# Kernel optimization log

Measured on AMD Instinct MI355X. Metric: run time of the kernel, lower is better.

The kernel has to match this reference:

```python
import jax, jax.numpy as jnp
import numpy as np

B, S, D = 1, 2048, 2048
E, K, F = 16, 4, 512
EPS = 1e-6


def setup_inputs() -> dict:
    key = jax.random.key(0)
    ks = jax.random.split(key, 5)
    return {
        "hidden_states": jax.random.normal(ks[0], (B, S, D), dtype=jnp.float32),
        "norm_weight": jnp.ones((D,), dtype=jnp.float32),
        "gate_w": jax.random.normal(ks[1], (E, D), dtype=jnp.float32) * 0.02,
        "w_gate": jax.random.normal(ks[2], (E, D, F), dtype=jnp.float32) * 0.02,
        "w_up": jax.random.normal(ks[3], (E, D, F), dtype=jnp.float32) * 0.02,
        "w_down": jax.random.normal(ks[4], (E, F, D), dtype=jnp.float32) * 0.02,
    }


def _rmsnorm(x, w, eps=EPS):
    xf = x.astype(jnp.float32)
    var = jnp.mean(xf * xf, axis=-1, keepdims=True)
    return (xf * jax.lax.rsqrt(var + eps)).astype(x.dtype) * w


def reference(hidden_states, norm_weight, gate_w, w_gate, w_up, w_down):
    residual = hidden_states
    h = _rmsnorm(hidden_states, norm_weight)
    x = h.reshape(-1, D)                                  # [T, D], T = B*S
    T = x.shape[0]

    # Router: softmax over experts (fp32), top-k, renormalize top-k weights.
    logits = x @ gate_w.T                                  # [T, E]
    probs = jax.nn.softmax(logits.astype(jnp.float32), axis=-1)
    top_w, top_i = jax.lax.top_k(probs, K)                 # [T, K]
    top_w = top_w / jnp.sum(top_w, axis=-1, keepdims=True)
    top_w = top_w.astype(x.dtype)

    # Dense combine matrix [T, E]: routing weight if selected, else 0.
    comb = jnp.zeros((T, E), dtype=x.dtype)
    comb = comb.at[jnp.arange(T)[:, None], top_i].add(top_w)

    # Experts: SiLU-gated MLP per expert, combined with routing weights.
    g = jnp.einsum("td,edf->tef", x, w_gate)               # [T, E, F]
    u = jnp.einsum("td,edf->tef", x, w_up)                 # [T, E, F]
    act = jax.nn.silu(g) * u                               # [T, E, F]
    # Weight per-expert contributions then project down.
    y = jnp.einsum("tef,efd,te->td", act, w_down, comb)    # [T, D]

    out = residual + y.reshape(B, S, D)
    return out
```

## Files before the change

kernel.cpp:

```cpp
#include <hip/hip_runtime.h>
#include <cstdint>
#include <cstddef>

#define T_ 2048
#define D_ 2048
#define E_ 16
#define F_ 512

typedef unsigned short u16;
typedef unsigned int u32;
typedef unsigned long long u64;
typedef __attribute__((ext_vector_type(8))) short bf16x8;
typedef __attribute__((ext_vector_type(4))) float f32x4;
typedef __attribute__((ext_vector_type(2))) u32 u32x2;
typedef __attribute__((ext_vector_type(8))) u16 u16x8;
typedef __attribute__((ext_vector_type(4))) u16 u16x4;

__device__ __forceinline__ u16 f2bf(float f){
  union { float f; u32 u; } c; c.f = f;
  return (u16)((c.u + 0x7FFFu + ((c.u >> 16) & 1u)) >> 16);
}

__device__ __forceinline__ void gload16(const void* g, void* l){
  __builtin_amdgcn_global_load_lds((const __attribute__((address_space(1))) void*)g,
                                   (__attribute__((address_space(3))) void*)l,
                                   16, 0, 0);
}

__device__ __forceinline__ void st4(u16* p, float4 v){
  u32 lo, hi;
  asm("v_cvt_pk_bf16_f32 %0, %1, %2" : "=v"(lo) : "v"(v.x), "v"(v.y));
  asm("v_cvt_pk_bf16_f32 %0, %1, %2" : "=v"(hi) : "v"(v.z), "v"(v.w));
  u32x2 u = {lo, hi};
  *(u32x2*)p = u;
}

__global__ __launch_bounds__(256) void k_transpose_cast(
    const float* __restrict__ src, u16* __restrict__ dst, int R, int C)
{
  const int e = blockIdx.z;
  const int r0 = blockIdx.y * 64, c0 = blockIdx.x * 64;
  const int tid = threadIdx.x;
  __shared__ __align__(16) u16 tile[64][68];
  const float* s = src + ((size_t)e * R + r0) * C + c0;
  const int ir = tid >> 4, jc = (tid & 15) * 4;
  #pragma unroll
  for (int q = 0; q < 4; ++q){
    const int i = ir + q*16;
    const float4 v = *(const float4*)(s + (size_t)i * C + jc);
    st4(&tile[i][jc], v);
  }
  __syncthreads();
  u16* d = dst + ((size_t)e * C + c0) * R + r0;
  #pragma unroll
  for (int q = 0; q < 4; ++q){
    const int a = ir + q*16;
    u16x4 pkt = { tile[jc+0][a], tile[jc+1][a], tile[jc+2][a], tile[jc+3][a] };
    *(u16x4*)(d + (size_t)a * R + jc) = pkt;
  }
}

__global__ __launch_bounds__(256) void k_norm_router(
    const float* __restrict__ x, const float* __restrict__ nw, const float* __restrict__ gw,
    u16* __restrict__ h, int* __restrict__ tok_e, float* __restrict__ tok_w)
{
  const int t = blockIdx.x, tid = threadIdx.x;
  const int lane = tid & 63, wid = tid >> 6;
  const int d0 = tid * 8;
  const float4 v0 = *(const float4*)(x + (size_t)t*D_ + d0);
  const float4 v1 = *(const float4*)(x + (size_t)t*D_ + d0 + 4);
  float hv[8] = {v0.x, v0.y, v0.z, v0.w, v1.x, v1.y, v1.z, v1.w};
  float ss = 0.f;
  #pragma unroll
  for (int j = 0; j < 8; ++j) ss += hv[j]*hv[j];
  #pragma unroll
  for (int o = 32; o; o >>= 1) ss += __shfl_xor(ss, o);
  __shared__ float sred[4];
  __shared__ float red16[4][16];
  __shared__ float lf[16];
  if (lane == 0) sred[wid] = ss;
  __syncthreads();
  const float rstd = rsqrtf((sred[0]+sred[1]+sred[2]+sred[3]) * (1.f/(float)D_) + 1e-6f);
  const float4 w0 = *(const float4*)(nw + d0);
  const float4 w1 = *(const float4*)(nw + d0 + 4);
  const float wv[8] = {w0.x,w0.y,w0.z,w0.w,w1.x,w1.y,w1.z,w1.w};
  #pragma unroll
  for (int j = 0; j < 8; ++j) hv[j] = hv[j] * rstd * wv[j];
  u16x8 hb;
  #pragma unroll
  for (int j = 0; j < 8; ++j) hb[j] = f2bf(hv[j]);
  *(u16x8*)(h + (size_t)t*D_ + d0) = hb;

  float lg[16];
  #pragma unroll
  for (int e = 0; e < 16; ++e){
    const float4 g0 = *(const float4*)(gw + e*D_ + d0);
    const float4 g1 = *(const float4*)(gw + e*D_ + d0 + 4);
    lg[e] = hv[0]*g0.x + hv[1]*g0.y + hv[2]*g0.z + hv[3]*g0.w
          + hv[4]*g1.x + hv[5]*g1.y + hv[6]*g1.z + hv[7]*g1.w;
  }
  #pragma unroll
  for (int e = 0; e < 16; ++e){
    #pragma unroll
    for (int o = 32; o; o >>= 1) lg[e] += __shfl_xor(lg[e], o);
  }
  if (lane == 0){
    #pragma unroll
    for (int e = 0; e < 16; ++e) red16[wid][e] = lg[e];
  }
  __syncthreads();
  if (tid < 16) lf[tid] = red16[0][tid] + red16[1][tid] + red16[2][tid] + red16[3][tid];
  __syncthreads();
  if (tid == 0){
    float l[16];
    #pragma unroll
    for (int e = 0; e < 16; ++e) l[e] = lf[e];
    int sel[4]; float sv[4]; u32 used = 0;
    for (int k = 0; k < 4; ++k){
      float b = -3.4e38f; int bi = 0;
      for (int e = 0; e < 16; ++e)
        if (!((used >> e) & 1u) && l[e] > b){ b = l[e]; bi = e; }
      used |= 1u << bi; sel[k] = bi; sv[k] = b;
    }
    float ex[4]; float s = 0.f;
    for (int k = 0; k < 4; ++k){ ex[k] = __expf(sv[k] - sv[0]); s += ex[k]; }
    const float inv = 1.f / s;
    int4 te = {sel[0], sel[1], sel[2], sel[3]};
    float4 tw4 = {ex[0]*inv, ex[1]*inv, ex[2]*inv, ex[3]*inv};
    *(int4*)(tok_e + t*4) = te;
    *(float4*)(tok_w + t*4) = tw4;
  }
}

__global__ __launch_bounds__(256) void k_build_lists(
    const int* __restrict__ tok_e, const float* __restrict__ tok_w,
    int* __restrict__ eidx, float* __restrict__ ew, int* __restrict__ counts)
{
  const int e = blockIdx.x, tid = threadIdx.x;
  const int lane = tid & 63, wid = tid >> 6;
  __shared__ int wtot[4];
  __shared__ int base;
  if (tid == 0) base = 0;
  __syncthreads();
  for (int t0 = 0; t0 < T_; t0 += 256){
    const int t = t0 + tid;
    const int4 te = *(const int4*)(tok_e + t*4);
    const float4 tw = *(const float4*)(tok_w + t*4);
    bool m = false; float wv = 0.f;
    if      (te.x == e){ m = true; wv = tw.x; }
    else if (te.y == e){ m = true; wv = tw.y; }
    else if (te.z == e){ m = true; wv = tw.z; }
    else if (te.w == e){ m = true; wv = tw.w; }
    const u64 mask = __ballot(m);
    const int pre = __popcll(mask & ((1ull << lane) - 1ull));
    if (lane == 0) wtot[wid] = __popcll(mask);
    __syncthreads();
    int wbase = base;
    for (int i = 0; i < wid; ++i) wbase += wtot[i];
    if (m){
      eidx[e*T_ + wbase + pre] = t;
      ew[e*T_ + wbase + pre] = wv;
    }
    __syncthreads();
    if (tid == 0) base += wtot[0] + wtot[1] + wtot[2] + wtot[3];
    __syncthreads();
  }
  if (tid == 0) counts[e] = base;
}

__global__ __launch_bounds__(256) void k_slots(
    const int* __restrict__ counts, const int* __restrict__ eidx,
    const int* __restrict__ tok_e, int* __restrict__ tok_slot)
{
  const int e = blockIdx.x;
  int abase = 0;
  for (int i = 0; i < e; ++i) abase += counts[i];
  const int cnt = counts[e];
  for (int s = threadIdx.x; s < cnt; s += 256){
    const int t = eidx[e*T_ + s];
    const int4 te = *(const int4*)(tok_e + t*4);
    const int kidx = (te.x == e) ? 0 : (te.y == e) ? 1 : (te.z == e) ? 2 : 3;
    tok_slot[t*4 + kidx] = abase + s;
  }
}

__global__ __launch_bounds__(256, 3) void k_gateup(
    const u16* __restrict__ h, const u16* __restrict__ wgT, const u16* __restrict__ wuT,
    const int* __restrict__ counts, const int* __restrict__ eidx, const float* __restrict__ ew,
    u16* __restrict__ act)
{
  const int bid = blockIdx.x;
  const int tt = bid >> 7;
  const int e  = (bid >> 3) & 15;
  const int ft = bid & 7;

  const int cnt = counts[e];
  const int row0 = tt * 128;
  if (row0 >= cnt) return;
  int abase = 0;
  for (int i = 0; i < e; ++i) abase += counts[i];

  const int tid = threadIdx.x, lane = tid & 63, w = tid >> 6;
  const int f0 = ft * 64;

  __shared__ __align__(16) u16 Xs[3][4096];
  __shared__ __align__(16) u16 Ws[3][4096];

  int* toksS = (int*)&Xs[0][0];
  if (tid < 128){
    const int slot = row0 + tid;
    const int cs = slot < cnt ? slot : (cnt - 1);
    toksS[tid] = eidx[e*T_ + cs];
  }
  __syncthreads();

  const int lr = lane >> 2, lc = lane & 3;
  const int csw = lc ^ (lr & 3) ^ (lr >> 2);

  const u16* srcX[2]; const u16* srcW[2]; u32 dof[2];
  #pragma unroll
  for (int q = 0; q < 2; ++q){
    const int r = w*32 + q*16 + lr;
    srcX[q] = h + (size_t)toksS[r]*D_ + 8*csw;
    const u16* wb = (r < 64) ? (wgT + ((size_t)e*F_ + f0 + r)*D_)
                             : (wuT + ((size_t)e*F_ + f0 + (r - 64))*D_);
    srcW[q] = wb + 8*csw;
    dof[q] = (u32)((w*32 + q*16) * 32);
  }
  __syncthreads();

  const int p = lane & 15, g4 = lane >> 4;
  const int tm = w >> 1, fh = w & 1;
  u32 aB[4], bB[4];
  #pragma unroll
  for (int m = 0; m < 4; ++m) aB[m] = (u32)((tm*64 + m*16 + p) * 32);
  #pragma unroll
  for (int n = 0; n < 2; ++n){
    bB[n]   = (u32)((     fh*32 + n*16 + p) * 32);
    bB[n+2] = (u32)((64 + fh*32 + n*16 + p) * 32);
  }
  const u32 s8 = 8u * (u32)(g4 ^ (p & 3) ^ (p >> 2));

  f32x4 acc[4][4] = {};

  #pragma unroll
  for (int b = 0; b < 2; ++b){
    const int kb = b * 32;
    #pragma unroll
    for (int q = 0; q < 2; ++q){
      gload16(srcX[q] + kb, (void*)&Xs[b][dof[q]]);
      gload16(srcW[q] + kb, (void*)&Ws[b][dof[q]]);
    }
  }

  const int NSTEP = D_ / 32;
  int cur = 0;
  for (int kt = 0; kt < NSTEP; ++kt){
    if (kt < NSTEP - 1) asm volatile("s_waitcnt vmcnt(4)" ::: "memory");
    else                asm volatile("s_waitcnt vmcnt(0)" ::: "memory");
    __builtin_amdgcn_sched_barrier(0);
    __builtin_amdgcn_s_barrier();
    __builtin_amdgcn_sched_barrier(0);
    if (kt + 2 < NSTEP){
      const int kb2 = (kt + 2) * 32;
      int nb = cur + 2; if (nb >= 3) nb -= 3;
      #pragma unroll
      for (int q = 0; q < 2; ++q){
        gload16(srcX[q] + kb2, (void*)&Xs[nb][dof[q]]);
        gload16(srcW[q] + kb2, (void*)&Ws[nb][dof[q]]);
      }
    }
    const u16* Xp = &Xs[cur][0];
    const u16* Wp = &Ws[cur][0];
    bf16x8 aF[4], bF[4];
    #pragma unroll
    for (int m = 0; m < 4; ++m) aF[m] = *(const bf16x8*)&Xp[aB[m] + s8];
    #pragma unroll
    for (int n = 0; n < 4; ++n) bF[n] = *(const bf16x8*)&Wp[bB[n] + s8];
    #pragma unroll
    for (int m = 0; m < 4; ++m)
      #pragma unroll
      for (int n = 0; n < 4; ++n)
        acc[m][n] = __builtin_amdgcn_mfma_f32_16x16x32_bf16(aF[m], bF[n], acc[m][n], 0, 0, 0);
    cur = (cur == 2) ? 0 : cur + 1;
  }

  #pragma unroll
  for (int m = 0; m < 4; ++m)
    #pragma unroll
    for (int r = 0; r < 4; ++r){
      const int row  = tm*64 + m*16 + g4*4 + r;
      const int slot = row0 + row;
      if (slot < cnt){
        const float tw = ew[e*T_ + slot];
        #pragma unroll
        for (int n = 0; n < 2; ++n){
          const float gv = acc[m][n][r], uv = acc[m][n+2][r];
          const float a = tw * (gv / (1.f + __expf(-gv))) * uv;
          act[(size_t)(abase + slot)*F_ + f0 + fh*32 + n*16 + p] = f2bf(a);
        }
      }
    }
}

__global__ __launch_bounds__(256, 3) void k_down(
    const u16* __restrict__ act, const u16* __restrict__ wdT,
    const int* __restrict__ counts, u16* __restrict__ ydown)
{
  const int bid = blockIdx.x;
  const int tt = bid >> 8;
  const int e  = (bid >> 4) & 15;
  const int dt = bid & 15;

  const int cnt = counts[e], row0 = tt * 128;
  if (row0 >= cnt) return;
  int abase = 0;
  for (int i = 0; i < e; ++i) abase += counts[i];

  const int tid = threadIdx.x, lane = tid & 63, w = tid >> 6;
  const int d0 = dt * 128;

  __shared__ __align__(16) u16 As[3][4096];
  __shared__ __align__(16) u16 Wd[3][4096];

  const int lr = lane >> 2, lc = lane & 3;
  const int csw = lc ^ (lr & 3) ^ (lr >> 2);

  const u16* srcX[2]; const u16* srcW[2]; u32 dof[2];
  #pragma unroll
  for (int q = 0; q < 2; ++q){
    const int r = w*32 + q*16 + lr;
    const int rs = (row0 + r < cnt) ? (row0 + r) : (cnt - 1);
    srcX[q] = act + (size_t)(abase + rs)*F_ + 8*csw;
    srcW[q] = wdT + ((size_t)e*D_ + d0 + r)*F_ + 8*csw;
    dof[q] = (u32)((w*32 + q*16) * 32);
  }

  const int p = lane & 15, g4 = lane >> 4;
  const int tm = w >> 1, dh = w & 1;
  u32 aB[4], bB[4];
  #pragma unroll
  for (int m = 0; m < 4; ++m) aB[m] = (u32)((tm*64 + m*16 + p) * 32);
  #pragma unroll
  for (int n = 0; n < 4; ++n) bB[n] = (u32)((dh*64 + n*16 + p) * 32);
  const u32 s8 = 8u * (u32)(g4 ^ (p & 3) ^ (p >> 2));

  f32x4 acc[4][4] = {};

  #pragma unroll
  for (int b = 0; b < 2; ++b){
    const int kb = b * 32;
    #pragma unroll
    for (int q = 0; q < 2; ++q){
      gload16(srcX[q] + kb, (void*)&As[b][dof[q]]);
      gload16(srcW[q] + kb, (void*)&Wd[b][dof[q]]);
    }
  }

  const int NSTEP = F_ / 32;
  int cur = 0;
  for (int kt = 0; kt < NSTEP; ++kt){
    if (kt < NSTEP - 1) asm volatile("s_waitcnt vmcnt(4)" ::: "memory");
    else                asm volatile("s_waitcnt vmcnt(0)" ::: "memory");
    __builtin_amdgcn_sched_barrier(0);
    __builtin_amdgcn_s_barrier();
    __builtin_amdgcn_sched_barrier(0);
    if (kt + 2 < NSTEP){
      const int kb2 = (kt + 2) * 32;
      int nb = cur + 2; if (nb >= 3) nb -= 3;
      #pragma unroll
      for (int q = 0; q < 2; ++q){
        gload16(srcX[q] + kb2, (void*)&As[nb][dof[q]]);
        gload16(srcW[q] + kb2, (void*)&Wd[nb][dof[q]]);
      }
    }
    const u16* Ap = &As[cur][0];
    const u16* Wp = &Wd[cur][0];
    bf16x8 aF[4], bF[4];
    #pragma unroll
    for (int m = 0; m < 4; ++m) aF[m] = *(const bf16x8*)&Ap[aB[m] + s8];
    #pragma unroll
    for (int n = 0; n < 4; ++n) bF[n] = *(const bf16x8*)&Wp[bB[n] + s8];
    #pragma unroll
    for (int m = 0; m < 4; ++m)
      #pragma unroll
      for (int n = 0; n < 4; ++n)
        acc[m][n] = __builtin_amdgcn_mfma_f32_16x16x32_bf16(aF[m], bF[n], acc[m][n], 0, 0, 0);
    cur = (cur == 2) ? 0 : cur + 1;
  }

  #pragma unroll
  for (int m = 0; m < 4; ++m){
    #pragma unroll
    for (int r = 0; r < 4; ++r){
      const int row  = tm*64 + m*16 + g4*4 + r;
      const int slot = row0 + row;
      if (slot < cnt){
        u16* yp = ydown + (size_t)(abase + slot)*D_ + d0 + dh*64;
        #pragma unroll
        for (int n = 0; n < 4; ++n)
          yp[n*16 + p] = f2bf(acc[m][n][r]);
      }
    }
  }
}

__global__ __launch_bounds__(256) void k_combine(
    const float* __restrict__ x, const u16* __restrict__ ydown,
    const int* __restrict__ tok_slot, float* __restrict__ out)
{
  const int t = blockIdx.x;
  const int d0 = threadIdx.x * 8;
  const int4 sl = *(const int4*)(tok_slot + t*4);
  const float4 x0 = *(const float4*)(x + (size_t)t*D_ + d0);
  const float4 x1 = *(const float4*)(x + (size_t)t*D_ + d0 + 4);
  float s[8] = {x0.x, x0.y, x0.z, x0.w, x1.x, x1.y, x1.z, x1.w};
  const int sls[4] = {sl.x, sl.y, sl.z, sl.w};
  #pragma unroll
  for (int k = 0; k < 4; ++k){
    const u16x8 v = *(const u16x8*)(ydown + (size_t)sls[k]*D_ + d0);
    #pragma unroll
    for (int j = 0; j < 8; ++j){
      union { u32 u; float f; } c; c.u = (u32)v[j] << 16;
      s[j] += c.f;
    }
  }
  float4 o0 = {s[0], s[1], s[2], s[3]};
  float4 o1 = {s[4], s[5], s[6], s[7]};
  *(float4*)(out + (size_t)t*D_ + d0)     = o0;
  *(float4*)(out + (size_t)t*D_ + d0 + 4) = o1;
}

extern "C" void kernel_launch(void* const* d_in, const int* in_sizes, int n_in,
                              void* d_out, int out_size, void* d_ws, size_t ws_size,
                              hipStream_t stream)
{
  (void)in_sizes; (void)n_in; (void)out_size; (void)ws_size;
  const float* x     = (const float*)d_in[0];
  const float* nw    = (const float*)d_in[1];
  const float* gw    = (const float*)d_in[2];
  const float* wgate = (const float*)d_in[3];
  const float* wup   = (const float*)d_in[4];
  const float* wdown = (const float*)d_in[5];
  float* out = (float*)d_out;

  char* ws = (char*)d_ws;
  u16*   h        = (u16*)(ws);
  u16*   act      = (u16*)(ws + 8388608);
  int*   counts   = (int*)(ws + 16908288);
  int*   eidx     = (int*)(ws + 16908352);
  float* ew       = (float*)(ws + 17039424);
  int*   tok_e    = (int*)(ws + 17170496);
  float* tok_w    = (float*)(ws + 17203264);
  int*   tok_slot = (int*)(ws + 17236032);
  u16*   wgT      = (u16*)(ws + 17268800);
  u16*   wuT      = (u16*)(ws + 50823232);
  u16*   wdT      = (u16*)(ws + 84377664);
  u16*   ydown    = (u16*)(ws + 17268800);

  k_transpose_cast<<<dim3(8, 32, 16), 256, 0, stream>>>(wgate, wgT, D_, F_);
  k_transpose_cast<<<dim3(8, 32, 16), 256, 0, stream>>>(wup,   wuT, D_, F_);
  k_transpose_cast<<<dim3(32, 8, 16), 256, 0, stream>>>(wdown, wdT, F_, D_);
  k_norm_router<<<T_, 256, 0, stream>>>(x, nw, gw, h, tok_e, tok_w);
  k_build_lists<<<E_, 256, 0, stream>>>(tok_e, tok_w, eidx, ew, counts);
  k_slots<<<E_, 256, 0, stream>>>(counts, eidx, tok_e, tok_slot);
  k_gateup<<<2048, 256, 0, stream>>>(h, wgT, wuT, counts, eidx, ew, act);
  k_down<<<4096, 256, 0, stream>>>(act, wdT, counts, ydown);
  k_combine<<<T_, 256, 0, stream>>>(x, ydown, tok_slot, out);
}
```

Measured before the change: 207.3 us.

## Halve expert GEMM row tiles to 64 and merge weight transposes into one launch

The gate/up and down expert GEMMs now use 64-token row tiles instead of 128. This halves the X/act LDS buffers and accumulator registers, doubles the grid and raises the occupancy hint to 4 blocks per CU. The aim is less wasted work on partially filled tiles for experts with uneven token counts, and more parallelism. The cost is that each weight tile is reused over fewer tokens, so weight traffic goes up. The three weight transpose-cast launches are also merged into one kernel to cut launch overhead.

```diff
diff --git a/kernel.cpp b/kernel.cpp
--- a/kernel.cpp
+++ b/kernel.cpp
@@ -35,11 +35,27 @@
   *(u32x2*)p = u;
 }
 
-__global__ __launch_bounds__(256) void k_transpose_cast(
-    const float* __restrict__ src, u16* __restrict__ dst, int R, int C)
-{
-  const int e = blockIdx.z;
-  const int r0 = blockIdx.y * 64, c0 = blockIdx.x * 64;
+__global__ __launch_bounds__(256) void k_transpose_all(
+    const float* __restrict__ wg, const float* __restrict__ wu, const float* __restrict__ wd,
+    u16* __restrict__ wgT, u16* __restrict__ wuT, u16* __restrict__ wdT)
+{
+  const int bid = blockIdx.x;
+  const int mat = bid >> 12;
+  const int rem = bid & 4095;
+  const int e = rem >> 8, within = rem & 255;
+  int R, C, r0, c0;
+  const float* src;
+  u16* dst;
+  if (mat < 2){
+    R = D_; C = F_;
+    r0 = (within >> 3) * 64;  c0 = (within & 7) * 64;
+    src = (mat == 0) ? wg : wu;
+    dst = (mat == 0) ? wgT : wuT;
+  } else {
+    R = F_; C = D_;
+    r0 = (within & 7) * 64;  c0 = (within >> 3) * 64;
+    src = wd; dst = wdT;
+  }
   const int tid = threadIdx.x;
   __shared__ __align__(16) u16 tile[64][68];
   const float* s = src + ((size_t)e * R + r0) * C + c0;
@@ -184,7 +200,7 @@
   }
 }
 
-__global__ __launch_bounds__(256, 3) void k_gateup(
+__global__ __launch_bounds__(256, 4) void k_gateup(
     const u16* __restrict__ h, const u16* __restrict__ wgT, const u16* __restrict__ wuT,
     const int* __restrict__ counts, const int* __restrict__ eidx, const float* __restrict__ ew,
     u16* __restrict__ act)
@@ -195,7 +211,7 @@
   const int ft = bid & 7;
 
   const int cnt = counts[e];
-  const int row0 = tt * 128;
+  const int row0 = tt * 64;
   if (row0 >= cnt) return;
   int abase = 0;
   for (int i = 0; i < e; ++i) abase += counts[i];
@@ -203,60 +219,54 @@
   const int tid = threadIdx.x, lane = tid & 63, w = tid >> 6;
   const int f0 = ft * 64;
 
-  __shared__ __align__(16) u16 Xs[3][4096];
+  __shared__ __align__(16) u16 Xs[3][2048];
   __shared__ __align__(16) u16 Ws[3][4096];
 
   int* toksS = (int*)&Xs[0][0];
-  if (tid < 128){
+  if (tid < 64){
     const int slot = row0 + tid;
     const int cs = slot < cnt ? slot : (cnt - 1);
     toksS[tid] = eidx[e*T_ + cs];
   }
   __syncthreads();
 
-  const int lr = lane >> 2, lc = lane & 3;
-  const int csw = lc ^ (lr & 3) ^ (lr >> 2);
-
-  const u16* srcX[2]; const u16* srcW[2]; u32 dof[2];
-  #pragma unroll
-  for (int q = 0; q < 2; ++q){
-    const int r = w*32 + q*16 + lr;
-    srcX[q] = h + (size_t)toksS[r]*D_ + 8*csw;
-    const u16* wb = (r < 64) ? (wgT + ((size_t)e*F_ + f0 + r)*D_)
-                             : (wuT + ((size_t)e*F_ + f0 + (r - 64))*D_);
-    srcW[q] = wb + 8*csw;
-    dof[q] = (u32)((w*32 + q*16) * 32);
-  }
+  const int r_ = tid >> 2, c_ = tid & 3;
+  const int csw = c_ ^ (r_ & 3) ^ ((r_ >> 2) & 3);
+
+  const u16* srcX  = h + (size_t)toksS[r_]*D_ + 8*csw;
+  const u16* srcW0 = wgT + ((size_t)e*F_ + f0 + r_)*D_ + 8*csw;
+  const u16* srcW1 = wuT + ((size_t)e*F_ + f0 + r_)*D_ + 8*csw;
+  const u32 dofX  = (u32)((w*16) * 32);
+  const u32 dofW0 = (u32)((w*16) * 32);
+  const u32 dofW1 = (u32)((64 + w*16) * 32);
   __syncthreads();
 
   const int p = lane & 15, g4 = lane >> 4;
   const int tm = w >> 1, fh = w & 1;
-  u32 aB[4], bB[4];
-  #pragma unroll
-  for (int m = 0; m < 4; ++m) aB[m] = (u32)((tm*64 + m*16 + p) * 32);
+  u32 aB[2], bB[4];
+  #pragma unroll
+  for (int m = 0; m < 2; ++m) aB[m] = (u32)((tm*32 + m*16 + p) * 32);
   #pragma unroll
   for (int n = 0; n < 2; ++n){
     bB[n]   = (u32)((     fh*32 + n*16 + p) * 32);
     bB[n+2] = (u32)((64 + fh*32 + n*16 + p) * 32);
   }
-  const u32 s8 = 8u * (u32)(g4 ^ (p & 3) ^ (p >> 2));
-
-  f32x4 acc[4][4] = {};
+  const u32 s8 = 8u * (u32)(g4 ^ (p & 3) ^ ((p >> 2) & 3));
+
+  f32x4 acc[2][4] = {};
 
   #pragma unroll
   for (int b = 0; b < 2; ++b){
     const int kb = b * 32;
-    #pragma unroll
-    for (int q = 0; q < 2; ++q){
-      gload16(srcX[q] + kb, (void*)&Xs[b][dof[q]]);
-      gload16(srcW[q] + kb, (void*)&Ws[b][dof[q]]);
-    }
+    gload16(srcX  + kb, (void*)&Xs[b][dofX]);
+    gload16(srcW0 + kb, (void*)&Ws[b][dofW0]);
+    gload16(srcW1 + kb, (void*)&Ws[b][dofW1]);
   }
 
   const int NSTEP = D_ / 32;
   int cur = 0;
   for (int kt = 0; kt < NSTEP; ++kt){
-    if (kt < NSTEP - 1) asm volatile("s_waitcnt vmcnt(4)" ::: "memory");
+    if (kt < NSTEP - 1) asm volatile("s_waitcnt vmcnt(3)" ::: "memory");
     else                asm volatile("s_waitcnt vmcnt(0)" ::: "memory");
     __builtin_amdgcn_sched_barrier(0);
     __builtin_amdgcn_s_barrier();
@@ -264,21 +274,19 @@
     if (kt + 2 < NSTEP){
       const int kb2 = (kt + 2) * 32;
       int nb = cur + 2; if (nb >= 3) nb -= 3;
-      #pragma unroll
-      for (int q = 0; q < 2; ++q){
-        gload16(srcX[q] + kb2, (void*)&Xs[nb][dof[q]]);
-        gload16(srcW[q] + kb2, (void*)&Ws[nb][dof[q]]);
-      }
+      gload16(srcX  + kb2, (void*)&Xs[nb][dofX]);
+      gload16(srcW0 + kb2, (void*)&Ws[nb][dofW0]);
+      gload16(srcW1 + kb2, (void*)&Ws[nb][dofW1]);
     }
     const u16* Xp = &Xs[cur][0];
     const u16* Wp = &Ws[cur][0];
-    bf16x8 aF[4], bF[4];
-    #pragma unroll
-    for (int m = 0; m < 4; ++m) aF[m] = *(const bf16x8*)&Xp[aB[m] + s8];
+    bf16x8 aF[2], bF[4];
+    #pragma unroll
+    for (int m = 0; m < 2; ++m) aF[m] = *(const bf16x8*)&Xp[aB[m] + s8];
     #pragma unroll
     for (int n = 0; n < 4; ++n) bF[n] = *(const bf16x8*)&Wp[bB[n] + s8];
     #pragma unroll
-    for (int m = 0; m < 4; ++m)
+    for (int m = 0; m < 2; ++m)
       #pragma unroll
       for (int n = 0; n < 4; ++n)
         acc[m][n] = __builtin_amdgcn_mfma_f32_16x16x32_bf16(aF[m], bF[n], acc[m][n], 0, 0, 0);
@@ -286,10 +294,10 @@
   }
 
   #pragma unroll
-  for (int m = 0; m < 4; ++m)
+  for (int m = 0; m < 2; ++m)
     #pragma unroll
     for (int r = 0; r < 4; ++r){
-      const int row  = tm*64 + m*16 + g4*4 + r;
+      const int row  = tm*32 + m*16 + g4*4 + r;
       const int slot = row0 + row;
       if (slot < cnt){
         const float tw = ew[e*T_ + slot];
@@ -303,7 +311,7 @@
     }
 }
 
-__global__ __launch_bounds__(256, 3) void k_down(
+__global__ __launch_bounds__(256, 4) void k_down(
     const u16* __restrict__ act, const u16* __restrict__ wdT,
     const int* __restrict__ counts, u16* __restrict__ ydown)
 {
@@ -312,7 +320,7 @@
   const int e  = (bid >> 4) & 15;
   const int dt = bid & 15;
 
-  const int cnt = counts[e], row0 = tt * 128;
+  const int cnt = counts[e], row0 = tt * 64;
   if (row0 >= cnt) return;
   int abase = 0;
   for (int i = 0; i < e; ++i) abase += counts[i];
@@ -320,47 +328,43 @@
   const int tid = threadIdx.x, lane = tid & 63, w = tid >> 6;
   const int d0 = dt * 128;
 
-  __shared__ __align__(16) u16 As[3][4096];
+  __shared__ __align__(16) u16 As[3][2048];
   __shared__ __align__(16) u16 Wd[3][4096];
 
-  const int lr = lane >> 2, lc = lane & 3;
-  const int csw = lc ^ (lr & 3) ^ (lr >> 2);
-
-  const u16* srcX[2]; const u16* srcW[2]; u32 dof[2];
-  #pragma unroll
-  for (int q = 0; q < 2; ++q){
-    const int r = w*32 + q*16 + lr;
-    const int rs = (row0 + r < cnt) ? (row0 + r) : (cnt - 1);
-    srcX[q] = act + (size_t)(abase + rs)*F_ + 8*csw;
-    srcW[q] = wdT + ((size_t)e*D_ + d0 + r)*F_ + 8*csw;
-    dof[q] = (u32)((w*32 + q*16) * 32);
-  }
+  const int r_ = tid >> 2, c_ = tid & 3;
+  const int csw = c_ ^ (r_ & 3) ^ ((r_ >> 2) & 3);
+
+  const int rs = (row0 + r_ < cnt) ? (row0 + r_) : (cnt - 1);
+  const u16* srcX  = act + (size_t)(abase + rs)*F_ + 8*csw;
+  const u16* srcW0 = wdT + ((size_t)e*D_ + d0 + r_)*F_ + 8*csw;
+  const u16* srcW1 = wdT + ((size_t)e*D_ + d0 + 64 + r_)*F_ + 8*csw;
+  const u32 dofX  = (u32)((w*16) * 32);
+  const u32 dofW0 = (u32)((w*16) * 32);
+  const u32 dofW1 = (u32)((64 + w*16) * 32);
 
   const int p = lane & 15, g4 = lane >> 4;
   const int tm = w >> 1, dh = w & 1;
-  u32 aB[4], bB[4];
-  #pragma unroll
-  for (int m = 0; m < 4; ++m) aB[m] = (u32)((tm*64 + m*16 + p) * 32);
+  u32 aB[2], bB[4];
+  #pragma unroll
+  for (int m = 0; m < 2; ++m) aB[m] = (u32)((tm*32 + m*16 + p) * 32);
   #pragma unroll
   for (int n = 0; n < 4; ++n) bB[n] = (u32)((dh*64 + n*16 + p) * 32);
-  const u32 s8 = 8u * (u32)(g4 ^ (p & 3) ^ (p >> 2));
-
-  f32x4 acc[4][4] = {};
+  const u32 s8 = 8u * (u32)(g4 ^ (p & 3) ^ ((p >> 2) & 3));
+
+  f32x4 acc[2][4] = {};
 
   #pragma unroll
   for (int b = 0; b < 2; ++b){
     const int kb = b * 32;
-    #pragma unroll
-    for (int q = 0; q < 2; ++q){
-      gload16(srcX[q] + kb, (void*)&As[b][dof[q]]);
-      gload16(srcW[q] + kb, (void*)&Wd[b][dof[q]]);
-    }
+    gload16(srcX  + kb, (void*)&As[b][dofX]);
+    gload16(srcW0 + kb, (void*)&Wd[b][dofW0]);
+    gload16(srcW1 + kb, (void*)&Wd[b][dofW1]);
   }
 
   const int NSTEP = F_ / 32;
   int cur = 0;
   for (int kt = 0; kt < NSTEP; ++kt){
-    if (kt < NSTEP - 1) asm volatile("s_waitcnt vmcnt(4)" ::: "memory");
+    if (kt < NSTEP - 1) asm volatile("s_waitcnt vmcnt(3)" ::: "memory");
     else                asm volatile("s_waitcnt vmcnt(0)" ::: "memory");
     __builtin_amdgcn_sched_barrier(0);
     __builtin_amdgcn_s_barrier();
@@ -368,21 +372,19 @@
     if (kt + 2 < NSTEP){
       const int kb2 = (kt + 2) * 32;
       int nb = cur + 2; if (nb >= 3) nb -= 3;
-      #pragma unroll
-      for (int q = 0; q < 2; ++q){
-        gload16(srcX[q] + kb2, (void*)&As[nb][dof[q]]);
-        gload16(srcW[q] + kb2, (void*)&Wd[nb][dof[q]]);
-      }
+      gload16(srcX  + kb2, (void*)&As[nb][dofX]);
+      gload16(srcW0 + kb2, (void*)&Wd[nb][dofW0]);
+      gload16(srcW1 + kb2, (void*)&Wd[nb][dofW1]);
     }
     const u16* Ap = &As[cur][0];
     const u16* Wp = &Wd[cur][0];
-    bf16x8 aF[4], bF[4];
-    #pragma unroll
-    for (int m = 0; m < 4; ++m) aF[m] = *(const bf16x8*)&Ap[aB[m] + s8];
+    bf16x8 aF[2], bF[4];
+    #pragma unroll
+    for (int m = 0; m < 2; ++m) aF[m] = *(const bf16x8*)&Ap[aB[m] + s8];
     #pragma unroll
     for (int n = 0; n < 4; ++n) bF[n] = *(const bf16x8*)&Wp[bB[n] + s8];
     #pragma unroll
-    for (int m = 0; m < 4; ++m)
+    for (int m = 0; m < 2; ++m)
       #pragma unroll
       for (int n = 0; n < 4; ++n)
         acc[m][n] = __builtin_amdgcn_mfma_f32_16x16x32_bf16(aF[m], bF[n], acc[m][n], 0, 0, 0);
@@ -390,10 +392,10 @@
   }
 
   #pragma unroll
-  for (int m = 0; m < 4; ++m){
+  for (int m = 0; m < 2; ++m){
     #pragma unroll
     for (int r = 0; r < 4; ++r){
-      const int row  = tm*64 + m*16 + g4*4 + r;
+      const int row  = tm*32 + m*16 + g4*4 + r;
       const int slot = row0 + row;
       if (slot < cnt){
         u16* yp = ydown + (size_t)(abase + slot)*D_ + d0 + dh*64;
@@ -458,13 +460,11 @@
   u16*   wdT      = (u16*)(ws + 84377664);
   u16*   ydown    = (u16*)(ws + 17268800);
 
-  k_transpose_cast<<<dim3(8, 32, 16), 256, 0, stream>>>(wgate, wgT, D_, F_);
-  k_transpose_cast<<<dim3(8, 32, 16), 256, 0, stream>>>(wup,   wuT, D_, F_);
-  k_transpose_cast<<<dim3(32, 8, 16), 256, 0, stream>>>(wdown, wdT, F_, D_);
+  k_transpose_all<<<12288, 256, 0, stream>>>(wgate, wup, wdown, wgT, wuT, wdT);
   k_norm_router<<<T_, 256, 0, stream>>>(x, nw, gw, h, tok_e, tok_w);
   k_build_lists<<<E_, 256, 0, stream>>>(tok_e, tok_w, eidx, ew, counts);
   k_slots<<<E_, 256, 0, stream>>>(counts, eidx, tok_e, tok_slot);
-  k_gateup<<<2048, 256, 0, stream>>>(h, wgT, wuT, counts, eidx, ew, act);
-  k_down<<<4096, 256, 0, stream>>>(act, wdT, counts, ydown);
+  k_gateup<<<4096, 256, 0, stream>>>(h, wgT, wuT, counts, eidx, ew, act);
+  k_down<<<8192, 256, 0, stream>>>(act, wdT, counts, ydown);
   k_combine<<<T_, 256, 0, stream>>>(x, ydown, tok_slot, out);
 }
```

Result: slower. 236.1 us (+13.9%).

## Use 2-wave 128-thread GEMM blocks with 64x128 per-wave tiles; merge transpose launches

Applied to the files above, without the earlier changes.

Rewrites the gate/up and down expert GEMM kernels to run with 128 threads (2 waves) per block instead of 4. Each wave now computes a 64x128 output tile with a 4x8 accumulator array, and each thread issues four async global-to-LDS loads per operand. The swizzle mask is adjusted to match. The goal is more MFMA work per LDS fragment load and fewer waves contending for the same tile, at the cost of more accumulator registers and lower occupancy. The three weight transpose/cast launches are also merged into one kernel to cut launch overhead.

```diff
diff --git a/kernel.cpp b/kernel.cpp
--- a/kernel.cpp
+++ b/kernel.cpp
@@ -35,11 +35,27 @@
   *(u32x2*)p = u;
 }
 
-__global__ __launch_bounds__(256) void k_transpose_cast(
-    const float* __restrict__ src, u16* __restrict__ dst, int R, int C)
-{
-  const int e = blockIdx.z;
-  const int r0 = blockIdx.y * 64, c0 = blockIdx.x * 64;
+__global__ __launch_bounds__(256) void k_transpose_all(
+    const float* __restrict__ wg, const float* __restrict__ wu, const float* __restrict__ wd,
+    u16* __restrict__ wgT, u16* __restrict__ wuT, u16* __restrict__ wdT)
+{
+  const int bid = blockIdx.x;
+  const int mat = bid >> 12;
+  const int rem = bid & 4095;
+  const int e = rem >> 8, within = rem & 255;
+  int R, C, r0, c0;
+  const float* src;
+  u16* dst;
+  if (mat < 2){
+    R = D_; C = F_;
+    r0 = (within >> 3) * 64;  c0 = (within & 7) * 64;
+    src = (mat == 0) ? wg : wu;
+    dst = (mat == 0) ? wgT : wuT;
+  } else {
+    R = F_; C = D_;
+    r0 = (within & 7) * 64;  c0 = (within >> 3) * 64;
+    src = wd; dst = wdT;
+  }
   const int tid = threadIdx.x;
   __shared__ __align__(16) u16 tile[64][68];
   const float* s = src + ((size_t)e * R + r0) * C + c0;
@@ -184,7 +200,7 @@
   }
 }
 
-__global__ __launch_bounds__(256, 3) void k_gateup(
+__global__ __launch_bounds__(128, 2) void k_gateup(
     const u16* __restrict__ h, const u16* __restrict__ wgT, const u16* __restrict__ wuT,
     const int* __restrict__ counts, const int* __restrict__ eidx, const float* __restrict__ ew,
     u16* __restrict__ act)
@@ -215,39 +231,35 @@
   __syncthreads();
 
   const int lr = lane >> 2, lc = lane & 3;
-  const int csw = lc ^ (lr & 3) ^ (lr >> 2);
-
-  const u16* srcX[2]; const u16* srcW[2]; u32 dof[2];
-  #pragma unroll
-  for (int q = 0; q < 2; ++q){
-    const int r = w*32 + q*16 + lr;
+  const int csw = lc ^ (lr & 3) ^ ((lr >> 2) & 3);
+
+  const u16* srcX[4]; const u16* srcW[4]; u32 dof[4];
+  #pragma unroll
+  for (int q = 0; q < 4; ++q){
+    const int r = w*64 + q*16 + lr;
     srcX[q] = h + (size_t)toksS[r]*D_ + 8*csw;
     const u16* wb = (r < 64) ? (wgT + ((size_t)e*F_ + f0 + r)*D_)
                              : (wuT + ((size_t)e*F_ + f0 + (r - 64))*D_);
     srcW[q] = wb + 8*csw;
-    dof[q] = (u32)((w*32 + q*16) * 32);
+    dof[q] = (u32)((w*64 + q*16) * 32);
   }
   __syncthreads();
 
   const int p = lane & 15, g4 = lane >> 4;
-  const int tm = w >> 1, fh = w & 1;
-  u32 aB[4], bB[4];
-  #pragma unroll
-  for (int m = 0; m < 4; ++m) aB[m] = (u32)((tm*64 + m*16 + p) * 32);
-  #pragma unroll
-  for (int n = 0; n < 2; ++n){
-    bB[n]   = (u32)((     fh*32 + n*16 + p) * 32);
-    bB[n+2] = (u32)((64 + fh*32 + n*16 + p) * 32);
-  }
-  const u32 s8 = 8u * (u32)(g4 ^ (p & 3) ^ (p >> 2));
-
-  f32x4 acc[4][4] = {};
+  u32 aB[4], bB[8];
+  #pragma unroll
+  for (int m = 0; m < 4; ++m) aB[m] = (u32)((w*64 + m*16 + p) * 32);
+  #pragma unroll
+  for (int n = 0; n < 8; ++n) bB[n] = (u32)((n*16 + p) * 32);
+  const u32 s8 = 8u * (u32)(g4 ^ (p & 3) ^ ((p >> 2) & 3));
+
+  f32x4 acc[4][8] = {};
 
   #pragma unroll
   for (int b = 0; b < 2; ++b){
     const int kb = b * 32;
     #pragma unroll
-    for (int q = 0; q < 2; ++q){
+    for (int q = 0; q < 4; ++q){
       gload16(srcX[q] + kb, (void*)&Xs[b][dof[q]]);
       gload16(srcW[q] + kb, (void*)&Ws[b][dof[q]]);
     }
@@ -256,7 +268,7 @@
   const int NSTEP = D_ / 32;
   int cur = 0;
   for (int kt = 0; kt < NSTEP; ++kt){
-    if (kt < NSTEP - 1) asm volatile("s_waitcnt vmcnt(4)" ::: "memory");
+    if (kt < NSTEP - 1) asm volatile("s_waitcnt vmcnt(8)" ::: "memory");
     else                asm volatile("s_waitcnt vmcnt(0)" ::: "memory");
     __builtin_amdgcn_sched_barrier(0);
     __builtin_amdgcn_s_barrier();
@@ -265,22 +277,22 @@
       const int kb2 = (kt + 2) * 32;
       int nb = cur + 2; if (nb >= 3) nb -= 3;
       #pragma unroll
-      for (int q = 0; q < 2; ++q){
+      for (int q = 0; q < 4; ++q){
         gload16(srcX[q] + kb2, (void*)&Xs[nb][dof[q]]);
         gload16(srcW[q] + kb2, (void*)&Ws[nb][dof[q]]);
       }
     }
     const u16* Xp = &Xs[cur][0];
     const u16* Wp = &Ws[cur][0];
-    bf16x8 aF[4], bF[4];
+    bf16x8 aF[4], bF[8];
     #pragma unroll
     for (int m = 0; m < 4; ++m) aF[m] = *(const bf16x8*)&Xp[aB[m] + s8];
     #pragma unroll
-    for (int n = 0; n < 4; ++n) bF[n] = *(const bf16x8*)&Wp[bB[n] + s8];
+    for (int n = 0; n < 8; ++n) bF[n] = *(const bf16x8*)&Wp[bB[n] + s8];
     #pragma unroll
     for (int m = 0; m < 4; ++m)
       #pragma unroll
-      for (int n = 0; n < 4; ++n)
+      for (int n = 0; n < 8; ++n)
         acc[m][n] = __builtin_amdgcn_mfma_f32_16x16x32_bf16(aF[m], bF[n], acc[m][n], 0, 0, 0);
     cur = (cur == 2) ? 0 : cur + 1;
   }
@@ -289,21 +301,21 @@
   for (int m = 0; m < 4; ++m)
     #pragma unroll
     for (int r = 0; r < 4; ++r){
-      const int row  = tm*64 + m*16 + g4*4 + r;
+      const int row  = w*64 + m*16 + g4*4 + r;
       const int slot = row0 + row;
       if (slot < cnt){
         const float tw = ew[e*T_ + slot];
         #pragma unroll
-        for (int n = 0; n < 2; ++n){
-          const float gv = acc[m][n][r], uv = acc[m][n+2][r];
+        for (int n = 0; n < 4; ++n){
+          const float gv = acc[m][n][r], uv = acc[m][n+4][r];
           const float a = tw * (gv / (1.f + __expf(-gv))) * uv;
-          act[(size_t)(abase + slot)*F_ + f0 + fh*32 + n*16 + p] = f2bf(a);
+          act[(size_t)(abase + slot)*F_ + f0 + n*16 + p] = f2bf(a);
         }
       }
     }
 }
 
-__global__ __launch_bounds__(256, 3) void k_down(
+__global__ __launch_bounds__(128, 2) void k_down(
     const u16* __restrict__ act, const u16* __restrict__ wdT,
     const int* __restrict__ counts, u16* __restrict__ ydown)
 {
@@ -324,34 +336,33 @@
   __shared__ __align__(16) u16 Wd[3][4096];
 
   const int lr = lane >> 2, lc = lane & 3;
-  const int csw = lc ^ (lr & 3) ^ (lr >> 2);
-
-  const u16* srcX[2]; const u16* srcW[2]; u32 dof[2];
-  #pragma unroll
-  for (int q = 0; q < 2; ++q){
-    const int r = w*32 + q*16 + lr;
+  const int csw = lc ^ (lr & 3) ^ ((lr >> 2) & 3);
+
+  const u16* srcX[4]; const u16* srcW[4]; u32 dof[4];
+  #pragma unroll
+  for (int q = 0; q < 4; ++q){
+    const int r = w*64 + q*16 + lr;
     const int rs = (row0 + r < cnt) ? (row0 + r) : (cnt - 1);
     srcX[q] = act + (size_t)(abase + rs)*F_ + 8*csw;
     srcW[q] = wdT + ((size_t)e*D_ + d0 + r)*F_ + 8*csw;
-    dof[q] = (u32)((w*32 + q*16) * 32);
+    dof[q] = (u32)((w*64 + q*16) * 32);
   }
 
   const int p = lane & 15, g4 = lane >> 4;
-  const int tm = w >> 1, dh = w & 1;
-  u32 aB[4], bB[4];
-  #pragma unroll
-  for (int m = 0; m < 4; ++m) aB[m] = (u32)((tm*64 + m*16 + p) * 32);
-  #pragma unroll
-  for (int n = 0; n < 4; ++n) bB[n] = (u32)((dh*64 + n*16 + p) * 32);
-  const u32 s8 = 8u * (u32)(g4 ^ (p & 3) ^ (p >> 2));
-
-  f32x4 acc[4][4] = {};
+  u32 aB[4], bB[8];
+  #pragma unroll
+  for (int m = 0; m < 4; ++m) aB[m] = (u32)((w*64 + m*16 + p) * 32);
+  #pragma unroll
+  for (int n = 0; n < 8; ++n) bB[n] = (u32)((n*16 + p) * 32);
+  const u32 s8 = 8u * (u32)(g4 ^ (p & 3) ^ ((p >> 2) & 3));
+
+  f32x4 acc[4][8] = {};
 
   #pragma unroll
   for (int b = 0; b < 2; ++b){
     const int kb = b * 32;
     #pragma unroll
-    for (int q = 0; q < 2; ++q){
+    for (int q = 0; q < 4; ++q){
       gload16(srcX[q] + kb, (void*)&As[b][dof[q]]);
       gload16(srcW[q] + kb, (void*)&Wd[b][dof[q]]);
     }
@@ -360,7 +371,7 @@
   const int NSTEP = F_ / 32;
   int cur = 0;
   for (int kt = 0; kt < NSTEP; ++kt){
-    if (kt < NSTEP - 1) asm volatile("s_waitcnt vmcnt(4)" ::: "memory");
+    if (kt < NSTEP - 1) asm volatile("s_waitcnt vmcnt(8)" ::: "memory");
     else                asm volatile("s_waitcnt vmcnt(0)" ::: "memory");
     __builtin_amdgcn_sched_barrier(0);
     __builtin_amdgcn_s_barrier();
@@ -369,22 +380,22 @@
       const int kb2 = (kt + 2) * 32;
       int nb = cur + 2; if (nb >= 3) nb -= 3;
       #pragma unroll
-      for (int q = 0; q < 2; ++q){
+      for (int q = 0; q < 4; ++q){
         gload16(srcX[q] + kb2, (void*)&As[nb][dof[q]]);
         gload16(srcW[q] + kb2, (void*)&Wd[nb][dof[q]]);
       }
     }
     const u16* Ap = &As[cur][0];
     const u16* Wp = &Wd[cur][0];
-    bf16x8 aF[4], bF[4];
+    bf16x8 aF[4], bF[8];
     #pragma unroll
     for (int m = 0; m < 4; ++m) aF[m] = *(const bf16x8*)&Ap[aB[m] + s8];
     #pragma unroll
-    for (int n = 0; n < 4; ++n) bF[n] = *(const bf16x8*)&Wp[bB[n] + s8];
+    for (int n = 0; n < 8; ++n) bF[n] = *(const bf16x8*)&Wp[bB[n] + s8];
     #pragma unroll
     for (int m = 0; m < 4; ++m)
       #pragma unroll
-      for (int n = 0; n < 4; ++n)
+      for (int n = 0; n < 8; ++n)
         acc[m][n] = __builtin_amdgcn_mfma_f32_16x16x32_bf16(aF[m], bF[n], acc[m][n], 0, 0, 0);
     cur = (cur == 2) ? 0 : cur + 1;
   }
@@ -393,12 +404,12 @@
   for (int m = 0; m < 4; ++m){
     #pragma unroll
     for (int r = 0; r < 4; ++r){
-      const int row  = tm*64 + m*16 + g4*4 + r;
+      const int row  = w*64 + m*16 + g4*4 + r;
       const int slot = row0 + row;
       if (slot < cnt){
-        u16* yp = ydown + (size_t)(abase + slot)*D_ + d0 + dh*64;
+        u16* yp = ydown + (size_t)(abase + slot)*D_ + d0;
         #pragma unroll
-        for (int n = 0; n < 4; ++n)
+        for (int n = 0; n < 8; ++n)
           yp[n*16 + p] = f2bf(acc[m][n][r]);
       }
     }
@@ -458,13 +469,11 @@
   u16*   wdT      = (u16*)(ws + 84377664);
   u16*   ydown    = (u16*)(ws + 17268800);
 
-  k_transpose_cast<<<dim3(8, 32, 16), 256, 0, stream>>>(wgate, wgT, D_, F_);
-  k_transpose_cast<<<dim3(8, 32, 16), 256, 0, stream>>>(wup,   wuT, D_, F_);
-  k_transpose_cast<<<dim3(32, 8, 16), 256, 0, stream>>>(wdown, wdT, F_, D_);
+  k_transpose_all<<<12288, 256, 0, stream>>>(wgate, wup, wdown, wgT, wuT, wdT);
   k_norm_router<<<T_, 256, 0, stream>>>(x, nw, gw, h, tok_e, tok_w);
   k_build_lists<<<E_, 256, 0, stream>>>(tok_e, tok_w, eidx, ew, counts);
   k_slots<<<E_, 256, 0, stream>>>(counts, eidx, tok_e, tok_slot);
-  k_gateup<<<2048, 256, 0, stream>>>(h, wgT, wuT, counts, eidx, ew, act);
-  k_down<<<4096, 256, 0, stream>>>(act, wdT, counts, ydown);
+  k_gateup<<<2048, 128, 0, stream>>>(h, wgT, wuT, counts, eidx, ew, act);
+  k_down<<<4096, 128, 0, stream>>>(act, wdT, counts, ydown);
   k_combine<<<T_, 256, 0, stream>>>(x, ydown, tok_slot, out);
 }
```

New measurement: 207.6 us. No clear change (+0.1%).
